# Kernel optimization log

Hardware: AMD Instinct MI355X
Metric: run time of the kernel (lower is better)

The kernel has to match this reference:

```python
import jax, jax.numpy as jnp
import numpy as np

B, NPG, HID, HEADS, L = 8, 512, 128, 8, 4
N = B * NPG
E = 16384
EDIM = HID // 4  # edge_dim = hidden_dim // 4 = 32


def _ln(x, g, b):
    m = x.mean(-1, keepdims=True)
    v = ((x - m) ** 2).mean(-1, keepdims=True)
    return (x - m) / jnp.sqrt(v + 1e-5) * g + b


def setup_inputs() -> dict:
    key = jax.random.key(0)
    ks = jax.random.split(key, 24)
    s = 0.05
    epg = E // B
    base = jnp.repeat(jnp.arange(B) * NPG, epg)
    src = base + jax.random.randint(ks[0], (E,), 0, NPG)
    dst = base + jax.random.randint(ks[1], (E,), 0, NPG)
    d = {
        'x': jax.random.randint(ks[2], (N, 1), 0, 100),
        'edge_index': jnp.stack([src, dst]),
        'edge_attr': jax.random.normal(ks[3], (E, 1), jnp.float32),
        'batch': jnp.repeat(jnp.arange(B), NPG),
        'atom_emb': jax.random.normal(ks[4], (100, HID)) * s,
        'edge_w': jax.random.normal(ks[5], (1, EDIM)) * s,
        'edge_b': jnp.zeros((EDIM,)),
        'wq': jax.random.normal(ks[6], (L, HID, HEADS * HID)) * s,
        'bq': jnp.zeros((L, HEADS * HID)),
        'wk': jax.random.normal(ks[7], (L, HID, HEADS * HID)) * s,
        'bk': jnp.zeros((L, HEADS * HID)),
        'wv': jax.random.normal(ks[8], (L, HID, HEADS * HID)) * s,
        'bv': jnp.zeros((L, HEADS * HID)),
        'we': jax.random.normal(ks[9], (L, EDIM, HEADS * HID)) * s,
        'wskip': jax.random.normal(ks[10], (L, HID, HID)) * s,
        'bskip': jnp.zeros((L, HID)),
        'ln_g': jnp.ones((L, HID)),
        'ln_b': jnp.zeros((L, HID)),
        'mha_in_w': jax.random.normal(ks[11], (HID, 3 * HID)) * s,
        'mha_in_b': jnp.zeros((3 * HID,)),
        'mha_out_w': jax.random.normal(ks[12], (HID, HID)) * s,
        'mha_out_b': jnp.zeros((HID,)),
        'w1': jax.random.normal(ks[13], (HID, HID)) * s,
        'b1': jnp.zeros((HID,)),
        'w2': jax.random.normal(ks[14], (HID, HID // 2)) * s,
        'b2': jnp.zeros((HID // 2,)),
        'w3': jax.random.normal(ks[15], (HID // 2, 3)) * s,
        'b3': jnp.zeros((3,)),
    }
    return d


def reference(x, edge_index, edge_attr, batch, atom_emb, edge_w, edge_b,
              wq, bq, wk, bk, wv, bv, we, wskip, bskip, ln_g, ln_b,
              mha_in_w, mha_in_b, mha_out_w, mha_out_b, w1, b1, w2, b2, w3, b3):
    src, dst = edge_index[0], edge_index[1]
    h = atom_emb[x[:, 0]]                       # [N, HID]
    e = edge_attr @ edge_w + edge_b             # [E, EDIM]
    scale = 1.0 / jnp.sqrt(jnp.float32(HID))    # per-head channel dim = HID
    for i in range(L):
        res = h
        q = (h @ wq[i] + bq[i]).reshape(N, HEADS, HID)
        k = (h @ wk[i] + bk[i]).reshape(N, HEADS, HID)
        v = (h @ wv[i] + bv[i]).reshape(N, HEADS, HID)
        ee = (e @ we[i]).reshape(E, HEADS, HID)
        kj = k[src] + ee                        # [E, HEADS, HID]
        vj = v[src] + ee
        logits = jnp.einsum('ehd,ehd->eh', q[dst], kj) * scale
        m = jax.ops.segment_max(logits, dst, num_segments=N)
        a = jnp.exp(logits - m[dst])
        z = jax.ops.segment_sum(a, dst, num_segments=N)
        a = a / (z[dst] + 1e-16)                # edge softmax per target node
        agg = jax.ops.segment_sum(a[:, :, None] * vj, dst, num_segments=N)
        out = agg.mean(axis=1) + h @ wskip[i] + bskip[i]  # concat=False + root skip
        h = jax.nn.gelu(_ln(out + res, ln_g[i], ln_b[i]), approximate=False)
    # equal-size graphs: ragged->padded conversion is a plain reshape, no padding
    p = h.reshape(B, NPG, HID)
    qkv = p @ mha_in_w + mha_in_b               # [B, n, 3*HID]
    hd = HID // HEADS
    q, k, v = [t.reshape(B, NPG, HEADS, hd).transpose(0, 2, 1, 3)
               for t in jnp.split(qkv, 3, axis=-1)]
    att = jax.nn.softmax(jnp.einsum('bhqd,bhkd->bhqk', q, k) / jnp.sqrt(jnp.float32(hd)), axis=-1)
    o = jnp.einsum('bhqk,bhkd->bhqd', att, v).transpose(0, 2, 1, 3).reshape(B, NPG, HID)
    o = (o @ mha_out_w + mha_out_b).reshape(N, HID)
    y = jax.nn.gelu(o @ w1 + b1, approximate=False)
    y = jax.nn.gelu(y @ w2 + b2, approximate=False)
    return y @ w3 + b3                          # [N, 3]
```

## Files before the change

### kernel.cpp

```cpp
#include <hip/hip_runtime.h>
#include <hip/hip_bf16.h>
#include <math.h>

#define NN 4096
#define NE 16384
#define NLAYERS 4

#define WT_STRIDE 442368

typedef __attribute__((ext_vector_type(8))) short bf16x8;
typedef __attribute__((ext_vector_type(4))) float floatx4;

__device__ __forceinline__ float gelu_f(float x) {
  return 0.5f * x * (1.0f + erff(x * 0.70710678118654752440f));
}

__device__ __forceinline__ void bsplit(float a, unsigned short& hi, unsigned short& lo) {
  __hip_bfloat16 h16 = __float2bfloat16(a);
  hi = *(unsigned short*)&h16;
  const float r = a - __bfloat162float(h16);
  __hip_bfloat16 l16 = __float2bfloat16(r);
  lo = *(unsigned short*)&l16;
}

union F16U { float4 v4[4]; float f[16]; };

__global__ void k_init(const int* __restrict__ x, const float* __restrict__ atom_emb,
                       const float* __restrict__ edge_attr, const float* __restrict__ edge_w,
                       const float* __restrict__ edge_b, float* __restrict__ h,
                       float* __restrict__ ef, int* __restrict__ counts,
                       unsigned short* __restrict__ hhi, unsigned short* __restrict__ hlo) {
  const int idx = blockIdx.x * 256 + threadIdx.x;
  const float hv = atom_emb[x[idx >> 7] * 128 + (idx & 127)];
  h[idx] = hv;
  bsplit(hv, hhi[idx], hlo[idx]);
  ef[idx] = edge_attr[idx >> 5] * edge_w[idx & 31] + edge_b[idx & 31];
  if (idx < NN) counts[idx] = 0;
}

__global__ void k_hist(const int* __restrict__ eidx, int* __restrict__ counts) {
  const int e = blockIdx.x * 256 + threadIdx.x;
  if (e < NE) atomicAdd(&counts[eidx[NE + e]], 1);
}

__global__ void k_scan(const int* __restrict__ counts, int* __restrict__ offs,
                       int* __restrict__ heads) {
  __shared__ int tmp[1024];
  const int t = threadIdx.x;
  const int c0 = counts[t*4], c1 = counts[t*4+1], c2 = counts[t*4+2], c3 = counts[t*4+3];
  const int s = c0 + c1 + c2 + c3;
  tmp[t] = s; __syncthreads();
  for (int off = 1; off < 1024; off <<= 1) {
    int v = (t >= off) ? tmp[t - off] : 0;
    __syncthreads();
    tmp[t] += v;
    __syncthreads();
  }
  int base = tmp[t] - s;
  offs[t*4]   = base;                heads[t*4]   = base;
  offs[t*4+1] = base + c0;           heads[t*4+1] = base + c0;
  offs[t*4+2] = base + c0 + c1;      heads[t*4+2] = base + c0 + c1;
  offs[t*4+3] = base + c0 + c1 + c2; heads[t*4+3] = base + c0 + c1 + c2;
  if (t == 1023) offs[NN] = tmp[1023];
}

__global__ void k_scatter(const int* __restrict__ eidx, int* __restrict__ heads,
                          int* __restrict__ elist) {
  const int e = blockIdx.x * 256 + threadIdx.x;
  if (e < NE) {
    int p = atomicAdd(&heads[eidx[NE + e]], 1);
    elist[p] = e;
  }
}

__global__ __launch_bounds__(256) void k_wcvt(
    const float* __restrict__ wq, const float* __restrict__ wk,
    const float* __restrict__ wv, const float* __restrict__ wsk,
    unsigned short* __restrict__ wthi, unsigned short* __restrict__ wtlo) {
  const int z = blockIdx.z;
  const int layer = z >> 2, mat = z & 3;
  int NC; const float* W; int woff;
  if (mat == 0)      { NC = 1024; W = wq  + (size_t)layer * 131072; woff = 0; }
  else if (mat == 1) { NC = 1024; W = wk  + (size_t)layer * 131072; woff = 131072; }
  else if (mat == 2) { NC = 1024; W = wv  + (size_t)layer * 131072; woff = 262144; }
  else               { NC = 128;  W = wsk + (size_t)layer * 16384;  woff = 393216; }
  const int c0 = blockIdx.x * 64;
  if (c0 >= NC) return;
  const int k0 = blockIdx.y * 64;
  __shared__ unsigned short th[64][65], tl[64][65];
  const int t = threadIdx.x;
  for (int i = t; i < 4096; i += 256) {
    const int kk = i >> 6, c = i & 63;
    bsplit(W[(size_t)(k0 + kk) * NC + c0 + c], th[kk][c], tl[kk][c]);
  }
  __syncthreads();
  unsigned short* oh = wthi + (size_t)layer * WT_STRIDE + woff;
  unsigned short* ol = wtlo + (size_t)layer * WT_STRIDE + woff;
  for (int i = t; i < 4096; i += 256) {
    const int n = i >> 6, k = i & 63;
    oh[(size_t)(c0 + n) * 128 + k0 + k] = th[k][n];
    ol[(size_t)(c0 + n) * 128 + k0 + k] = tl[k][n];
  }
}

__global__ __launch_bounds__(256) void k_wqe(
    const float* __restrict__ wq, const float* __restrict__ bq,
    const float* __restrict__ we, unsigned short* __restrict__ wthi,
    unsigned short* __restrict__ wtlo, float* __restrict__ bqe) {
  const int layer = blockIdx.x >> 3, hh = blockIdx.x & 7;
  const float* wq_l = wq + (size_t)layer * 131072;
  const float* we_l = we + (size_t)layer * 32768;
  const float* bq_l = bq + (size_t)layer * 1024;
  __shared__ float wqS[128][132];
  __shared__ float weS[32][132];
  const int t = threadIdx.x;
  for (int i = t; i < 4096; i += 256) {
    const int d = i >> 5, dd4 = (i & 31) << 2;
    *(float4*)&wqS[d][dd4] = *(const float4*)&wq_l[(size_t)d * 1024 + hh * 128 + dd4];
  }
  for (int i = t; i < 1024; i += 256) {
    const int c = i >> 5, dd4 = (i & 31) << 2;
    *(float4*)&weS[c][dd4] = *(const float4*)&we_l[(size_t)c * 1024 + hh * 128 + dd4];
  }
  __syncthreads();
  const int d = t & 127, cg = t >> 7;
  float acc[16];
  #pragma unroll
  for (int cc = 0; cc < 16; cc++) acc[cc] = 0.f;
  for (int dd = 0; dd < 128; dd++) {
    const float a = wqS[d][dd];
    #pragma unroll
    for (int cc = 0; cc < 16; cc++)
      acc[cc] += a * weS[cg * 16 + cc][dd];
  }
  unsigned short* oh = wthi + (size_t)layer * WT_STRIDE + 409600;
  unsigned short* ol = wtlo + (size_t)layer * WT_STRIDE + 409600;
  #pragma unroll
  for (int cc = 0; cc < 16; cc++) {
    const int j = hh * 32 + cg * 16 + cc;
    unsigned short hi, lo;
    bsplit(acc[cc], hi, lo);
    oh[(size_t)j * 128 + d] = hi;
    ol[(size_t)j * 128 + d] = lo;
  }
  if (t < 32) {
    float s = 0.f;
    for (int dd = 0; dd < 128; dd++) s += bq_l[hh * 128 + dd] * weS[t][dd];
    bqe[layer * 256 + hh * 32 + t] = s;
  }
}

__global__ __launch_bounds__(256) void k_mfqkv(
    const unsigned short* __restrict__ hhi, const unsigned short* __restrict__ hlo,
    const unsigned short* __restrict__ wth, const unsigned short* __restrict__ wtl,
    const float* __restrict__ bq, const float* __restrict__ bk,
    const float* __restrict__ bv, const float* __restrict__ bsk,
    const float* __restrict__ bqe_l,
    float* __restrict__ qb, float* __restrict__ kb,
    float* __restrict__ vb, float* __restrict__ skb, float* __restrict__ qeb) {
  const int xb = blockIdx.x;
  int NC; const float* bias; float* C; int woff; int c0;
  if (xb < 16)      { NC = 1024; bias = bq;    C = qb;  woff = 0;      c0 = xb * 64; }
  else if (xb < 32) { NC = 1024; bias = bk;    C = kb;  woff = 131072; c0 = (xb-16) * 64; }
  else if (xb < 48) { NC = 1024; bias = bv;    C = vb;  woff = 262144; c0 = (xb-32) * 64; }
  else if (xb < 50) { NC = 128;  bias = bsk;   C = skb; woff = 393216; c0 = (xb-48) * 64; }
  else              { NC = 256;  bias = bqe_l; C = qeb; woff = 409600; c0 = (xb-50) * 64; }
  __shared__ unsigned short Ah[64][136], Al[64][136], Wh[64][136], Wl[64][136];
  const int t = threadIdx.x;
  const int n0 = blockIdx.y * 64;
  for (int i = t; i < 1024; i += 256) {
    const int r = i >> 4, c8 = (i & 15) << 3;
    *(uint4*)&Ah[r][c8] = *(const uint4*)&hhi[(size_t)(n0 + r) * 128 + c8];
    *(uint4*)&Al[r][c8] = *(const uint4*)&hlo[(size_t)(n0 + r) * 128 + c8];
    *(uint4*)&Wh[r][c8] = *(const uint4*)&wth[woff + (size_t)(c0 + r) * 128 + c8];
    *(uint4*)&Wl[r][c8] = *(const uint4*)&wtl[woff + (size_t)(c0 + r) * 128 + c8];
  }
  __syncthreads();
  const int w = t >> 6, l = t & 63;
  const int quad = l >> 4, lm = l & 15;
  floatx4 acc[4] = {{0.f,0.f,0.f,0.f},{0.f,0.f,0.f,0.f},{0.f,0.f,0.f,0.f},{0.f,0.f,0.f,0.f}};
  #pragma unroll
  for (int kc = 0; kc < 4; kc++) {
    const int ko = kc * 32 + quad * 8;
    const bf16x8 ah = *(const bf16x8*)&Ah[w * 16 + lm][ko];
    const bf16x8 al = *(const bf16x8*)&Al[w * 16 + lm][ko];
    #pragma unroll
    for (int ct = 0; ct < 4; ct++) {
      const bf16x8 bh = *(const bf16x8*)&Wh[ct * 16 + lm][ko];
      const bf16x8 bl = *(const bf16x8*)&Wl[ct * 16 + lm][ko];
      acc[ct] = __builtin_amdgcn_mfma_f32_16x16x32_bf16(ah, bh, acc[ct], 0, 0, 0);
      acc[ct] = __builtin_amdgcn_mfma_f32_16x16x32_bf16(ah, bl, acc[ct], 0, 0, 0);
      acc[ct] = __builtin_amdgcn_mfma_f32_16x16x32_bf16(al, bh, acc[ct], 0, 0, 0);
    }
  }
  #pragma unroll
  for (int ct = 0; ct < 4; ct++) {
    const int col = c0 + ct * 16 + lm;
    const float bb = bias[col];
    #pragma unroll
    for (int r = 0; r < 4; r++) {
      const int row = n0 + w * 16 + quad * 4 + r;
      C[(size_t)row * NC + col] = acc[ct][r] + bb;
    }
  }
}

__global__ __launch_bounds__(256) void k_gemm2(const float* __restrict__ A,
                                               const float* __restrict__ W,
                                               const float* __restrict__ bias,
                                               float* __restrict__ C, int NC, int gelu) {
  __shared__ float As[128][65];
  __shared__ float Ws[128][64];
  const int t = threadIdx.x;
  const int n0 = blockIdx.y * 64, c0 = blockIdx.x * 64;
  for (int i = t; i < 2048; i += 256) {
    const int r = i & 63, k4 = (i >> 6) << 2;
    const float4 a = *(const float4*)&A[(size_t)(n0 + r) * 128 + k4];
    As[k4+0][r] = a.x; As[k4+1][r] = a.y; As[k4+2][r] = a.z; As[k4+3][r] = a.w;
  }
  for (int i = t; i < 2048; i += 256) {
    const int kk = i >> 4, c4 = (i & 15) << 2;
    *(float4*)&Ws[kk][c4] = *(const float4*)&W[(size_t)kk * NC + c0 + c4];
  }
  __syncthreads();
  const int tr = (t >> 4) << 2;
  const int tc = (t & 15) << 2;
  float acc[4][4];
  #pragma unroll
  for (int i = 0; i < 4; i++)
    #pragma unroll
    for (int j = 0; j < 4; j++) acc[i][j] = 0.f;
  #pragma unroll 8
  for (int k = 0; k < 128; k++) {
    const float4 av = *(const float4*)&As[k][tr];
    const float4 wv = *(const float4*)&Ws[k][tc];
    acc[0][0] += av.x*wv.x; acc[0][1] += av.x*wv.y; acc[0][2] += av.x*wv.z; acc[0][3] += av.x*wv.w;
    acc[1][0] += av.y*wv.x; acc[1][1] += av.y*wv.y; acc[1][2] += av.y*wv.z; acc[1][3] += av.y*wv.w;
    acc[2][0] += av.z*wv.x; acc[2][1] += av.z*wv.y; acc[2][2] += av.z*wv.z; acc[2][3] += av.z*wv.w;
    acc[3][0] += av.w*wv.x; acc[3][1] += av.w*wv.y; acc[3][2] += av.w*wv.z; acc[3][3] += av.w*wv.w;
  }
  const float4 bb = *(const float4*)&bias[c0 + tc];
  #pragma unroll
  for (int i = 0; i < 4; i++) {
    float4 v;
    v.x = acc[i][0] + bb.x; v.y = acc[i][1] + bb.y;
    v.z = acc[i][2] + bb.z; v.w = acc[i][3] + bb.w;
    if (gelu) { v.x = gelu_f(v.x); v.y = gelu_f(v.y); v.z = gelu_f(v.z); v.w = gelu_f(v.w); }
    *(float4*)&C[(size_t)(n0 + tr + i) * NC + c0 + tc] = v;
  }
}

__global__ __launch_bounds__(512) void k_edgepost(
    const float* __restrict__ qb, const float* __restrict__ kb,
    const float* __restrict__ vb, const float* __restrict__ qe,
    const float* __restrict__ ef, const int* __restrict__ offs,
    const int* __restrict__ elist, const int* __restrict__ eidx,
    const float* __restrict__ we_l, const float* __restrict__ skb,
    const float* __restrict__ lng, const float* __restrict__ lnb,
    float* __restrict__ h,
    unsigned short* __restrict__ hhi, unsigned short* __restrict__ hlo) {
  __shared__ float Ss[8][256];
  __shared__ float Am[8][128];
  const int t = threadIdx.x;
  const int wid = t >> 6, lane = t & 63;
  const int n0 = (blockIdx.x & 7) * 512 + (blockIdx.x >> 3) * 8;
  const int n = n0 + wid;
  {
    const int hh = lane >> 3, s8 = lane & 7;
    const int d0 = hh * 128 + s8 * 16;
    F16U qv;
    {
      const float4* qp = (const float4*)(qb + (size_t)n * 1024 + d0);
      #pragma unroll
      for (int i = 0; i < 4; i++) qv.v4[i] = qp[i];
    }
    const float4 qe4 = *(const float4*)(qe + (size_t)n * 256 + hh * 32 + s8 * 4);
    float m = -INFINITY, z = 0.f;
    float acc[16];
    #pragma unroll
    for (int i = 0; i < 16; i++) acc[i] = 0.f;
    float sx = 0.f, sy = 0.f, sz = 0.f, sw = 0.f;
    const int e0 = offs[n], e1 = offs[n + 1];
    for (int tt = e0; tt < e1; tt++) {
      const int e = elist[tt];
      const int src = eidx[e];
      F16U kv;
      {
        const float4* kp = (const float4*)(kb + (size_t)src * 1024 + d0);
        #pragma unroll
        for (int i = 0; i < 4; i++) kv.v4[i] = kp[i];
      }
      const float4 ef4 = *(const float4*)(ef + (size_t)e * 32 + s8 * 4);
      float p0 = qe4.x*ef4.x + qe4.y*ef4.y;
      float p1 = qe4.z*ef4.z + qe4.w*ef4.w;
      float p2 = 0.f, p3 = 0.f;
      #pragma unroll
      for (int i = 0; i < 4; i++) {
        p0 += qv.f[i]      * kv.f[i];
        p1 += qv.f[4 + i]  * kv.f[4 + i];
        p2 += qv.f[8 + i]  * kv.f[8 + i];
        p3 += qv.f[12 + i] * kv.f[12 + i];
      }
      float p = (p0 + p1) + (p2 + p3);
      p += __shfl_xor(p, 1);
      p += __shfl_xor(p, 2);
      p += __shfl_xor(p, 4);
      const float logit = p * 0.08838834764831845f;
      if (logit > m + 8.f) {
        const float f = __expf(m - logit);
        z *= f; sx *= f; sy *= f; sz *= f; sw *= f;
        #pragma unroll
        for (int i = 0; i < 16; i++) acc[i] *= f;
        m = logit;
      }
      const float w = __expf(logit - m);
      z += w;
      F16U vv;
      {
        const float4* vp = (const float4*)(vb + (size_t)src * 1024 + d0);
        #pragma unroll
        for (int i = 0; i < 4; i++) vv.v4[i] = vp[i];
      }
      #pragma unroll
      for (int i = 0; i < 16; i++) acc[i] += w * vv.f[i];
      sx += w * ef4.x; sy += w * ef4.y;
      sz += w * ef4.z; sw += w * ef4.w;
    }
    const float inv = 1.f / (z + 1e-16f);
    *(float4*)&Ss[wid][hh * 32 + s8 * 4] =
        make_float4(sx * inv, sy * inv, sz * inv, sw * inv);
    F16U ov;
    #pragma unroll
    for (int i = 0; i < 16; i++) ov.f[i] = acc[i] * inv;
    #pragma unroll
    for (int mask = 8; mask <= 32; mask <<= 1)
      #pragma unroll
      for (int i = 0; i < 16; i++) ov.f[i] += __shfl_xor(ov.f[i], mask);
    if (hh == 0) {
      #pragma unroll
      for (int i = 0; i < 16; i++) ov.f[i] *= 0.125f;
      #pragma unroll
      for (int i = 0; i < 4; i++)
        *(float4*)&Am[wid][s8 * 16 + i * 4] = ov.v4[i];
    }
  }
  __syncthreads();
  {
    const int col = t & 127, grp = t >> 7;
    float acc0 = 0.f, acc1 = 0.f;
    const float* wp = we_l + col;
    #pragma unroll
    for (int hh2 = 0; hh2 < 8; hh2++) {
      #pragma unroll 4
      for (int c = 0; c < 32; c++) {
        const float wv = wp[(size_t)c * 1024 + hh2 * 128];
        const int k = hh2 * 32 + c;
        acc0 += Ss[grp * 2 + 0][k] * wv;
        acc1 += Ss[grp * 2 + 1][k] * wv;
      }
    }
    const int nA = grp * 2, nB = grp * 2 + 1;
    const size_t oA = (size_t)(n0 + nA) * 128 + col;
    const size_t oB = (size_t)(n0 + nB) * 128 + col;
    Am[nA][col] = Am[nA][col] + 0.125f * acc0 + skb[oA] + h[oA];
    Am[nB][col] = Am[nB][col] + 0.125f * acc1 + skb[oB] + h[oB];
  }
  __syncthreads();
  {
    const float v0 = Am[wid][lane], v1 = Am[wid][lane + 64];
    float s = v0 + v1;
    #pragma unroll
    for (int mask = 1; mask <= 32; mask <<= 1) s += __shfl_xor(s, mask);
    const float mean = s * (1.f / 128.f);
    const float d0 = v0 - mean, d1 = v1 - mean;
    float q = d0 * d0 + d1 * d1;
    #pragma unroll
    for (int mask = 1; mask <= 32; mask <<= 1) q += __shfl_xor(q, mask);
    const float rstd = 1.f / sqrtf(q * (1.f / 128.f) + 1e-5f);
    const float y0 = d0 * rstd * lng[lane] + lnb[lane];
    const float y1 = d1 * rstd * lng[lane + 64] + lnb[lane + 64];
    const float r0 = gelu_f(y0);
    const float r1 = gelu_f(y1);
    const size_t o = (size_t)n * 128 + lane;
    h[o] = r0;
    h[o + 64] = r1;
    bsplit(r0, hhi[o], hlo[o]);
    bsplit(r1, hhi[o + 64], hlo[o + 64]);
  }
}

__global__ __launch_bounds__(256) void k_attn2b(const float* __restrict__ qkvm,
                                                float* __restrict__ pm,
                                                float* __restrict__ pz,
                                                float* __restrict__ pacc) {
  __shared__ float ks2[64][16];
  __shared__ float vs2[64][16];
  const int ksp = blockIdx.x, qt = blockIdx.y, bh = blockIdx.z;
  const int b = bh >> 3, hh = bh & 7;
  const int t = threadIdx.x;
  const size_t rbase = (size_t)(b * 512 + ksp * 64);
  {
    const int j = t >> 2, d4 = (t & 3) << 2;
    const size_t ro = (rbase + j) * 384 + hh * 16 + d4;
    *(float4*)&ks2[j][d4] = *(const float4*)&qkvm[ro + 128];
    *(float4*)&vs2[j][d4] = *(const float4*)&qkvm[ro + 256];
  }
  __syncthreads();
  const int qrow = qt * 256 + t;
  const int nq = b * 512 + qrow;
  F16U qv;
  {
    const float4* qp = (const float4*)(qkvm + (size_t)nq * 384 + hh * 16);
    #pragma unroll
    for (int i = 0; i < 4; i++) qv.v4[i] = qp[i];
  }
  float m = -INFINITY, z = 0.f;
  float acc[16];
  #pragma unroll
  for (int i = 0; i < 16; i++) acc[i] = 0.f;
  for (int j = 0; j < 64; j += 2) {
    F16U k0, k1, v0, v1;
    {
      const float4* p0 = (const float4*)ks2[j];
      const float4* p1 = (const float4*)ks2[j + 1];
      const float4* q0 = (const float4*)vs2[j];
      const float4* q1 = (const float4*)vs2[j + 1];
      #pragma unroll
      for (int i = 0; i < 4; i++) {
        k0.v4[i] = p0[i]; k1.v4[i] = p1[i];
        v0.v4[i] = q0[i]; v1.v4[i] = q1[i];
      }
    }
    float a0 = 0.f, a1 = 0.f, a2 = 0.f, a3 = 0.f;
    float b0 = 0.f, b1 = 0.f, b2 = 0.f, b3 = 0.f;
    #pragma unroll
    for (int i = 0; i < 4; i++) {
      a0 += qv.f[i]      * k0.f[i];
      a1 += qv.f[4 + i]  * k0.f[4 + i];
      a2 += qv.f[8 + i]  * k0.f[8 + i];
      a3 += qv.f[12 + i] * k0.f[12 + i];
      b0 += qv.f[i]      * k1.f[i];
      b1 += qv.f[4 + i]  * k1.f[4 + i];
      b2 += qv.f[8 + i]  * k1.f[8 + i];
      b3 += qv.f[12 + i] * k1.f[12 + i];
    }
    const float sa = ((a0 + a1) + (a2 + a3)) * 0.25f;
    const float sb = ((b0 + b1) + (b2 + b3)) * 0.25f;
    const float smax = fmaxf(sa, sb);
    if (smax > m + 8.f) {
      const float f = __expf(m - smax);
      z *= f;
      #pragma unroll
      for (int i = 0; i < 16; i++) acc[i] *= f;
      m = smax;
    }
    const float wa = __expf(sa - m);
    const float wb = __expf(sb - m);
    z += wa + wb;
    #pragma unroll
    for (int i = 0; i < 16; i++)
      acc[i] += wa * v0.f[i] + wb * v1.f[i];
  }
  const int p = (bh * 512 + qrow) * 8 + ksp;
  pm[p] = m; pz[p] = z;
  float4* pp = (float4*)&pacc[(size_t)p * 16];
  F16U ov;
  #pragma unroll
  for (int i = 0; i < 16; i++) ov.f[i] = acc[i];
  #pragma unroll
  for (int i = 0; i < 4; i++) pp[i] = ov.v4[i];
}

__global__ __launch_bounds__(256) void k_tail(
    const float* __restrict__ pm, const float* __restrict__ pz,
    const float* __restrict__ pacc,
    const float* __restrict__ mha_out_w, const float* __restrict__ mha_out_b,
    const float* __restrict__ w1, const float* __restrict__ b1,
    const float* __restrict__ w2, const float* __restrict__ b2,
    const float* __restrict__ w3, const float* __restrict__ b3,
    float* __restrict__ out) {
  __shared__ float RA[4][128];
  __shared__ float RB[4][128];
  const int t = threadIdx.x;
  const int w = t >> 6, lane = t & 63;
  const int n = blockIdx.x * 4 + w;
  const int b = n >> 9, qrow = n & 511;
  #pragma unroll
  for (int half = 0; half < 2; half++) {
    const int c = lane + half * 64;
    const int hh = c >> 4, d = c & 15;
    const int base = ((b * 8 + hh) * 512 + qrow) * 8;
    float ms = pm[base];
    #pragma unroll
    for (int s = 1; s < 8; s++) ms = fmaxf(ms, pm[base + s]);
    float z = 0.f, o = 0.f;
    #pragma unroll
    for (int s = 0; s < 8; s++) {
      const float wg = __expf(pm[base + s] - ms);
      z += pz[base + s] * wg;
      o += pacc[(size_t)(base + s) * 16 + d] * wg;
    }
    RA[w][c] = o / z;
  }
  __syncthreads();
  {
    float a0 = 0.f, a1 = 0.f;
    #pragma unroll 8
    for (int k = 0; k < 128; k++) {
      const float r = RA[w][k];
      a0 += r * mha_out_w[k * 128 + lane];
      a1 += r * mha_out_w[k * 128 + lane + 64];
    }
    RB[w][lane]      = a0 + mha_out_b[lane];
    RB[w][lane + 64] = a1 + mha_out_b[lane + 64];
  }
  __syncthreads();
  {
    float a0 = 0.f, a1 = 0.f;
    #pragma unroll 8
    for (int k = 0; k < 128; k++) {
      const float r = RB[w][k];
      a0 += r * w1[k * 128 + lane];
      a1 += r * w1[k * 128 + lane + 64];
    }
    RA[w][lane]      = gelu_f(a0 + b1[lane]);
    RA[w][lane + 64] = gelu_f(a1 + b1[lane + 64]);
  }
  __syncthreads();
  {
    float a0 = 0.f;
    #pragma unroll 8
    for (int k = 0; k < 128; k++)
      a0 += RA[w][k] * w2[k * 64 + lane];
    RB[w][lane] = gelu_f(a0 + b2[lane]);
  }
  __syncthreads();
  if (lane < 3) {
    float s = b3[lane];
    for (int c = 0; c < 64; c++) s += RB[w][c] * w3[c * 3 + lane];
    out[(size_t)n * 3 + lane] = s;
  }
}

extern "C" void kernel_launch(void* const* d_in, const int* in_sizes, int n_in,
                              void* d_out, int out_size, void* d_ws, size_t ws_size,
                              hipStream_t stream) {
  const int*   x         = (const int*)d_in[0];
  const int*   eidx      = (const int*)d_in[1];
  const float* edge_attr = (const float*)d_in[2];
  const float* atom_emb  = (const float*)d_in[4];
  const float* edge_w    = (const float*)d_in[5];
  const float* edge_b    = (const float*)d_in[6];
  const float* wq        = (const float*)d_in[7];
  const float* bq        = (const float*)d_in[8];
  const float* wk        = (const float*)d_in[9];
  const float* bk        = (const float*)d_in[10];
  const float* wv        = (const float*)d_in[11];
  const float* bv        = (const float*)d_in[12];
  const float* we        = (const float*)d_in[13];
  const float* wskip     = (const float*)d_in[14];
  const float* bskip     = (const float*)d_in[15];
  const float* ln_g      = (const float*)d_in[16];
  const float* ln_b      = (const float*)d_in[17];
  const float* mha_in_w  = (const float*)d_in[18];
  const float* mha_in_b  = (const float*)d_in[19];
  const float* mha_out_w = (const float*)d_in[20];
  const float* mha_out_b = (const float*)d_in[21];
  const float* w1        = (const float*)d_in[22];
  const float* b1        = (const float*)d_in[23];
  const float* w2        = (const float*)d_in[24];
  const float* b2        = (const float*)d_in[25];
  const float* w3        = (const float*)d_in[26];
  const float* b3        = (const float*)d_in[27];

  float* ws   = (float*)d_ws;
  float* h    = ws;
  float* ef   = h + 524288;
  float* qb   = ef + 524288;
  float* kb   = qb + 4194304;
  float* vb   = kb + 4194304;
  float* qe   = vb + 4194304;
  float* big  = qe + 1048576;
  float* skb  = big + 1048576;
  unsigned short* hhi  = (unsigned short*)(big + 1572864);
  unsigned short* hlo  = hhi + 524288;
  unsigned short* wthi = hlo + 524288;
  unsigned short* wtlo = wthi + 1769472;
  float* sbuf = big + 4194304;
  float* qkvm = qb;
  float* pm   = sbuf;
  float* pz   = sbuf + 262144;
  float* pacc = big;
  int* counts = (int*)(sbuf + 1048576);
  int* offs   = counts + 4100;
  int* heads  = offs + 4100;
  int* elist  = heads + 4100;
  float* bqe  = (float*)(elist + 16384);

  k_init<<<2048, 256, 0, stream>>>(x, atom_emb, edge_attr, edge_w, edge_b, h, ef, counts,
                                   hhi, hlo);
  k_hist<<<64, 256, 0, stream>>>(eidx, counts);
  k_scan<<<1, 1024, 0, stream>>>(counts, offs, heads);
  k_scatter<<<64, 256, 0, stream>>>(eidx, heads, elist);
  k_wcvt<<<dim3(16, 2, 16), 256, 0, stream>>>(wq, wk, wv, wskip, wthi, wtlo);
  k_wqe<<<32, 256, 0, stream>>>(wq, bq, we, wthi, wtlo, bqe);

  for (int i = 0; i < NLAYERS; i++) {
    const float* bq_i  = bq + (size_t)i * 1024;
    const float* bk_i  = bk + (size_t)i * 1024;
    const float* bv_i  = bv + (size_t)i * 1024;
    const float* we_i  = we + (size_t)i * 32768;
    const float* bsk_i = bskip + (size_t)i * 128;
    const float* g_i   = ln_g + (size_t)i * 128;
    const float* b_i   = ln_b + (size_t)i * 128;
    const unsigned short* wth_i = wthi + (size_t)i * WT_STRIDE;
    const unsigned short* wtl_i = wtlo + (size_t)i * WT_STRIDE;

    k_mfqkv<<<dim3(54, 64), 256, 0, stream>>>(hhi, hlo, wth_i, wtl_i,
                                              bq_i, bk_i, bv_i, bsk_i, bqe + i * 256,
                                              qb, kb, vb, skb, qe);
    k_edgepost<<<512, 512, 0, stream>>>(qb, kb, vb, qe, ef, offs, elist, eidx,
                                        we_i, skb, g_i, b_i, h, hhi, hlo);
  }

  k_gemm2<<<dim3(6, 64), 256, 0, stream>>>(h, mha_in_w, mha_in_b, qkvm, 384, 0);
  k_attn2b<<<dim3(8, 2, 64), 256, 0, stream>>>(qkvm, pm, pz, pacc);
  k_tail<<<1024, 256, 0, stream>>>(pm, pz, pacc,
                                   mha_out_w, mha_out_b, w1, b1, w2, b2, w3, b3,
                                   (float*)d_out);
}
```

Measured before the change: 478.7 us.

## Fuse CSR scatter into scan, split attention keys finer, tile tail MLP weights

Merges the edge scatter into the single-block scan kernel, using shared-memory atomics for the per-node heads and dropping one launch. Doubles the attention key-split count (16 chunks of 32 keys) to raise block count and parallelism, at the cost of more partial results for the tail to merge. Restructures the tail MLP so each block handles 8 rows and stages weight tiles in shared memory, reusing each weight load across two rows per warp. Partial buffers move to the kb region to fit the larger split.

```diff
diff --git a/kernel.cpp b/kernel.cpp
--- a/kernel.cpp
+++ b/kernel.cpp
@@ -43,9 +43,10 @@
   if (e < NE) atomicAdd(&counts[eidx[NE + e]], 1);
 }
 
-__global__ void k_scan(const int* __restrict__ counts, int* __restrict__ offs,
-                       int* __restrict__ heads) {
+__global__ void k_scan2(const int* __restrict__ counts, int* __restrict__ offs,
+                        const int* __restrict__ eidx, int* __restrict__ elist) {
   __shared__ int tmp[1024];
+  __shared__ int sheads[4096];
   const int t = threadIdx.x;
   const int c0 = counts[t*4], c1 = counts[t*4+1], c2 = counts[t*4+2], c3 = counts[t*4+3];
   const int s = c0 + c1 + c2 + c3;
@@ -57,18 +58,14 @@
     __syncthreads();
   }
   int base = tmp[t] - s;
-  offs[t*4]   = base;                heads[t*4]   = base;
-  offs[t*4+1] = base + c0;           heads[t*4+1] = base + c0;
-  offs[t*4+2] = base + c0 + c1;      heads[t*4+2] = base + c0 + c1;
-  offs[t*4+3] = base + c0 + c1 + c2; heads[t*4+3] = base + c0 + c1 + c2;
+  offs[t*4]   = base;                sheads[t*4]   = base;
+  offs[t*4+1] = base + c0;           sheads[t*4+1] = base + c0;
+  offs[t*4+2] = base + c0 + c1;      sheads[t*4+2] = base + c0 + c1;
+  offs[t*4+3] = base + c0 + c1 + c2; sheads[t*4+3] = base + c0 + c1 + c2;
   if (t == 1023) offs[NN] = tmp[1023];
-}
-
-__global__ void k_scatter(const int* __restrict__ eidx, int* __restrict__ heads,
-                          int* __restrict__ elist) {
-  const int e = blockIdx.x * 256 + threadIdx.x;
-  if (e < NE) {
-    int p = atomicAdd(&heads[eidx[NE + e]], 1);
+  __syncthreads();
+  for (int e = t; e < NE; e += 1024) {
+    const int p = atomicAdd(&sheads[eidx[NE + e]], 1);
     elist[p] = e;
   }
 }
@@ -393,17 +390,17 @@
                                                 float* __restrict__ pm,
                                                 float* __restrict__ pz,
                                                 float* __restrict__ pacc) {
-  __shared__ float ks2[64][16];
-  __shared__ float vs2[64][16];
+  __shared__ float ks2[32][16];
+  __shared__ float vs2[32][16];
   const int ksp = blockIdx.x, qt = blockIdx.y, bh = blockIdx.z;
   const int b = bh >> 3, hh = bh & 7;
   const int t = threadIdx.x;
-  const size_t rbase = (size_t)(b * 512 + ksp * 64);
-  {
-    const int j = t >> 2, d4 = (t & 3) << 2;
+  const size_t rbase = (size_t)(b * 512 + ksp * 32);
+  {
+    const int j = (t & 127) >> 2, d4 = (t & 3) << 2;
     const size_t ro = (rbase + j) * 384 + hh * 16 + d4;
-    *(float4*)&ks2[j][d4] = *(const float4*)&qkvm[ro + 128];
-    *(float4*)&vs2[j][d4] = *(const float4*)&qkvm[ro + 256];
+    if (t < 128) *(float4*)&ks2[j][d4] = *(const float4*)&qkvm[ro + 128];
+    else         *(float4*)&vs2[j][d4] = *(const float4*)&qkvm[ro + 256];
   }
   __syncthreads();
   const int qrow = qt * 256 + t;
@@ -418,7 +415,7 @@
   float acc[16];
   #pragma unroll
   for (int i = 0; i < 16; i++) acc[i] = 0.f;
-  for (int j = 0; j < 64; j += 2) {
+  for (int j = 0; j < 32; j += 2) {
     F16U k0, k1, v0, v1;
     {
       const float4* p0 = (const float4*)ks2[j];
@@ -461,7 +458,7 @@
     for (int i = 0; i < 16; i++)
       acc[i] += wa * v0.f[i] + wb * v1.f[i];
   }
-  const int p = (bh * 512 + qrow) * 8 + ksp;
+  const int p = (bh * 512 + qrow) * 16 + ksp;
   pm[p] = m; pz[p] = z;
   float4* pp = (float4*)&pacc[(size_t)p * 16];
   F16U ov;
@@ -479,66 +476,121 @@
     const float* __restrict__ w2, const float* __restrict__ b2,
     const float* __restrict__ w3, const float* __restrict__ b3,
     float* __restrict__ out) {
-  __shared__ float RA[4][128];
-  __shared__ float RB[4][128];
+  __shared__ float R0[8][128];
+  __shared__ float R1[8][128];
+  __shared__ float Wc[32][128];
   const int t = threadIdx.x;
   const int w = t >> 6, lane = t & 63;
-  const int n = blockIdx.x * 4 + w;
-  const int b = n >> 9, qrow = n & 511;
-  #pragma unroll
-  for (int half = 0; half < 2; half++) {
-    const int c = lane + half * 64;
-    const int hh = c >> 4, d = c & 15;
-    const int base = ((b * 8 + hh) * 512 + qrow) * 8;
-    float ms = pm[base];
-    #pragma unroll
-    for (int s = 1; s < 8; s++) ms = fmaxf(ms, pm[base + s]);
-    float z = 0.f, o = 0.f;
-    #pragma unroll
-    for (int s = 0; s < 8; s++) {
-      const float wg = __expf(pm[base + s] - ms);
-      z += pz[base + s] * wg;
-      o += pacc[(size_t)(base + s) * 16 + d] * wg;
-    }
-    RA[w][c] = o / z;
-  }
-  __syncthreads();
+  const int n0 = blockIdx.x * 8;
+  const int r0i = w * 2, r1i = w * 2 + 1;
+  #pragma unroll
+  for (int rr = 0; rr < 2; rr++) {
+    const int n = n0 + w * 2 + rr;
+    const int b = n >> 9, qrow = n & 511;
+    #pragma unroll
+    for (int half = 0; half < 2; half++) {
+      const int c = lane + half * 64;
+      const int hh = c >> 4, d = c & 15;
+      const int base = ((b * 8 + hh) * 512 + qrow) * 16;
+      float ms = pm[base];
+      #pragma unroll
+      for (int s = 1; s < 16; s++) ms = fmaxf(ms, pm[base + s]);
+      float z = 0.f, o = 0.f;
+      #pragma unroll
+      for (int s = 0; s < 16; s++) {
+        const float wg = __expf(pm[base + s] - ms);
+        z += pz[base + s] * wg;
+        o += pacc[(size_t)(base + s) * 16 + d] * wg;
+      }
+      R0[w * 2 + rr][c] = o / z;
+    }
+  }
+  {
+    float a00 = 0.f, a01 = 0.f, a10 = 0.f, a11 = 0.f;
+    for (int kc = 0; kc < 4; kc++) {
+      __syncthreads();
+      #pragma unroll
+      for (int i = 0; i < 4; i++) {
+        const int idx = i * 256 + t, kk = idx >> 5, c4 = (idx & 31) << 2;
+        *(float4*)&Wc[kk][c4] = *(const float4*)&mha_out_w[(size_t)(kc*32 + kk) * 128 + c4];
+      }
+      __syncthreads();
+      for (int k4 = 0; k4 < 32; k4 += 4) {
+        const float4 rv0 = *(const float4*)&R0[r0i][kc*32 + k4];
+        const float4 rv1 = *(const float4*)&R0[r1i][kc*32 + k4];
+        #pragma unroll
+        for (int j = 0; j < 4; j++) {
+          const float wv0 = Wc[k4 + j][lane], wv1 = Wc[k4 + j][lane + 64];
+          const float rr0 = ((const float*)&rv0)[j], rr1 = ((const float*)&rv1)[j];
+          a00 += rr0 * wv0; a01 += rr0 * wv1;
+          a10 += rr1 * wv0; a11 += rr1 * wv1;
+        }
+      }
+    }
+    R1[r0i][lane]      = a00 + mha_out_b[lane];
+    R1[r0i][lane + 64] = a01 + mha_out_b[lane + 64];
+    R1[r1i][lane]      = a10 + mha_out_b[lane];
+    R1[r1i][lane + 64] = a11 + mha_out_b[lane + 64];
+  }
+  {
+    float a00 = 0.f, a01 = 0.f, a10 = 0.f, a11 = 0.f;
+    for (int kc = 0; kc < 4; kc++) {
+      __syncthreads();
+      #pragma unroll
+      for (int i = 0; i < 4; i++) {
+        const int idx = i * 256 + t, kk = idx >> 5, c4 = (idx & 31) << 2;
+        *(float4*)&Wc[kk][c4] = *(const float4*)&w1[(size_t)(kc*32 + kk) * 128 + c4];
+      }
+      __syncthreads();
+      for (int k4 = 0; k4 < 32; k4 += 4) {
+        const float4 rv0 = *(const float4*)&R1[r0i][kc*32 + k4];
+        const float4 rv1 = *(const float4*)&R1[r1i][kc*32 + k4];
+        #pragma unroll
+        for (int j = 0; j < 4; j++) {
+          const float wv0 = Wc[k4 + j][lane], wv1 = Wc[k4 + j][lane + 64];
+          const float rr0 = ((const float*)&rv0)[j], rr1 = ((const float*)&rv1)[j];
+          a00 += rr0 * wv0; a01 += rr0 * wv1;
+          a10 += rr1 * wv0; a11 += rr1 * wv1;
+        }
+      }
+    }
+    R0[r0i][lane]      = gelu_f(a00 + b1[lane]);
+    R0[r0i][lane + 64] = gelu_f(a01 + b1[lane + 64]);
+    R0[r1i][lane]      = gelu_f(a10 + b1[lane]);
+    R0[r1i][lane + 64] = gelu_f(a11 + b1[lane + 64]);
+  }
   {
     float a0 = 0.f, a1 = 0.f;
-    #pragma unroll 8
-    for (int k = 0; k < 128; k++) {
-      const float r = RA[w][k];
-      a0 += r * mha_out_w[k * 128 + lane];
-      a1 += r * mha_out_w[k * 128 + lane + 64];
-    }
-    RB[w][lane]      = a0 + mha_out_b[lane];
-    RB[w][lane + 64] = a1 + mha_out_b[lane + 64];
-  }
-  __syncthreads();
-  {
-    float a0 = 0.f, a1 = 0.f;
-    #pragma unroll 8
-    for (int k = 0; k < 128; k++) {
-      const float r = RB[w][k];
-      a0 += r * w1[k * 128 + lane];
-      a1 += r * w1[k * 128 + lane + 64];
-    }
-    RA[w][lane]      = gelu_f(a0 + b1[lane]);
-    RA[w][lane + 64] = gelu_f(a1 + b1[lane + 64]);
-  }
-  __syncthreads();
-  {
-    float a0 = 0.f;
-    #pragma unroll 8
-    for (int k = 0; k < 128; k++)
-      a0 += RA[w][k] * w2[k * 64 + lane];
-    RB[w][lane] = gelu_f(a0 + b2[lane]);
-  }
-  __syncthreads();
+    for (int kc = 0; kc < 4; kc++) {
+      __syncthreads();
+      #pragma unroll
+      for (int i = 0; i < 2; i++) {
+        const int idx = i * 256 + t, kk = idx >> 4, c4 = (idx & 15) << 2;
+        *(float4*)&Wc[kk][c4] = *(const float4*)&w2[(size_t)(kc*32 + kk) * 64 + c4];
+      }
+      __syncthreads();
+      for (int k4 = 0; k4 < 32; k4 += 4) {
+        const float4 rv0 = *(const float4*)&R0[r0i][kc*32 + k4];
+        const float4 rv1 = *(const float4*)&R0[r1i][kc*32 + k4];
+        #pragma unroll
+        for (int j = 0; j < 4; j++) {
+          const float wv = Wc[k4 + j][lane];
+          a0 += ((const float*)&rv0)[j] * wv;
+          a1 += ((const float*)&rv1)[j] * wv;
+        }
+      }
+    }
+    R1[r0i][lane] = gelu_f(a0 + b2[lane]);
+    R1[r1i][lane] = gelu_f(a1 + b2[lane]);
+  }
   if (lane < 3) {
-    float s = b3[lane];
-    for (int c = 0; c < 64; c++) s += RB[w][c] * w3[c * 3 + lane];
-    out[(size_t)n * 3 + lane] = s;
+    #pragma unroll
+    for (int rr = 0; rr < 2; rr++) {
+      const int row = w * 2 + rr;
+      float s = b3[lane];
+      for (int c = 0; c < 64; c++) s += R1[row][c] * w3[c * 3 + lane];
+      out[(size_t)(n0 + row) * 3 + lane] = s;
+    }
   }
 }
 
@@ -589,8 +641,8 @@
   float* sbuf = big + 4194304;
   float* qkvm = qb;
   float* pm   = sbuf;
-  float* pz   = sbuf + 262144;
-  float* pacc = big;
+  float* pz   = sbuf + 524288;
+  float* pacc = kb;
   int* counts = (int*)(sbuf + 1048576);
   int* offs   = counts + 4100;
   int* heads  = offs + 4100;
@@ -600,8 +652,7 @@
   k_init<<<2048, 256, 0, stream>>>(x, atom_emb, edge_attr, edge_w, edge_b, h, ef, counts,
                                    hhi, hlo);
   k_hist<<<64, 256, 0, stream>>>(eidx, counts);
-  k_scan<<<1, 1024, 0, stream>>>(counts, offs, heads);
-  k_scatter<<<64, 256, 0, stream>>>(eidx, heads, elist);
+  k_scan2<<<1, 1024, 0, stream>>>(counts, offs, eidx, elist);
   k_wcvt<<<dim3(16, 2, 16), 256, 0, stream>>>(wq, wk, wv, wskip, wthi, wtlo);
   k_wqe<<<32, 256, 0, stream>>>(wq, bq, we, wthi, wtlo, bqe);
 
@@ -624,8 +675,8 @@
   }
 
   k_gemm2<<<dim3(6, 64), 256, 0, stream>>>(h, mha_in_w, mha_in_b, qkvm, 384, 0);
-  k_attn2b<<<dim3(8, 2, 64), 256, 0, stream>>>(qkvm, pm, pz, pacc);
-  k_tail<<<1024, 256, 0, stream>>>(pm, pz, pacc,
-                                   mha_out_w, mha_out_b, w1, b1, w2, b2, w3, b3,
-                                   (float*)d_out);
-}
+  k_attn2b<<<dim3(16, 2, 64), 256, 0, stream>>>(qkvm, pm, pz, pacc);
+  k_tail<<<512, 256, 0, stream>>>(pm, pz, pacc,
+                                  mha_out_w, mha_out_b, w1, b1, w2, b2, w3, b3,
+                                  (float*)d_out);
+}
```

Result: slower. 521.7 us (+9.0%).

## Fuse CSR scan with scatter and register-block MLP tail over transposed weights

Applied to the files above, without the earlier changes.

The scan kernel now also scatters edges into the CSR list, using bucket heads kept in shared memory, which removes one launch and the global atomics. A new setup kernel stores transposed copies of the MHA out-projection, w1 and w2. The tail kernel then has each wave handle two rows, reads weight rows as float4 and reuses each weight load for both rows. Block-level barriers in the tail are dropped because each wave only touches its own rows. The per-lane strided reads of the transposed weights are not coalesced and depend on cache hits.

```diff
diff --git a/kernel.cpp b/kernel.cpp
--- a/kernel.cpp
+++ b/kernel.cpp
@@ -43,9 +43,10 @@
   if (e < NE) atomicAdd(&counts[eidx[NE + e]], 1);
 }
 
-__global__ void k_scan(const int* __restrict__ counts, int* __restrict__ offs,
-                       int* __restrict__ heads) {
+__global__ void k_scan2(const int* __restrict__ counts, int* __restrict__ offs,
+                        const int* __restrict__ eidx, int* __restrict__ elist) {
   __shared__ int tmp[1024];
+  __shared__ int sheads[4096];
   const int t = threadIdx.x;
   const int c0 = counts[t*4], c1 = counts[t*4+1], c2 = counts[t*4+2], c3 = counts[t*4+3];
   const int s = c0 + c1 + c2 + c3;
@@ -57,18 +58,14 @@
     __syncthreads();
   }
   int base = tmp[t] - s;
-  offs[t*4]   = base;                heads[t*4]   = base;
-  offs[t*4+1] = base + c0;           heads[t*4+1] = base + c0;
-  offs[t*4+2] = base + c0 + c1;      heads[t*4+2] = base + c0 + c1;
-  offs[t*4+3] = base + c0 + c1 + c2; heads[t*4+3] = base + c0 + c1 + c2;
+  offs[t*4]   = base;                sheads[t*4]   = base;
+  offs[t*4+1] = base + c0;           sheads[t*4+1] = base + c0;
+  offs[t*4+2] = base + c0 + c1;      sheads[t*4+2] = base + c0 + c1;
+  offs[t*4+3] = base + c0 + c1 + c2; sheads[t*4+3] = base + c0 + c1 + c2;
   if (t == 1023) offs[NN] = tmp[1023];
-}
-
-__global__ void k_scatter(const int* __restrict__ eidx, int* __restrict__ heads,
-                          int* __restrict__ elist) {
-  const int e = blockIdx.x * 256 + threadIdx.x;
-  if (e < NE) {
-    int p = atomicAdd(&heads[eidx[NE + e]], 1);
+  __syncthreads();
+  for (int e = t; e < NE; e += 1024) {
+    const int p = atomicAdd(&sheads[eidx[NE + e]], 1);
     elist[p] = e;
   }
 }
@@ -147,6 +144,21 @@
     float s = 0.f;
     for (int dd = 0; dd < 128; dd++) s += bq_l[hh * 128 + dd] * weS[t][dd];
     bqe[layer * 256 + hh * 32 + t] = s;
+  }
+}
+
+__global__ void k_wt(const float* __restrict__ mo, const float* __restrict__ w1,
+                     const float* __restrict__ w2, float* __restrict__ wtT) {
+  const int idx = blockIdx.x * 256 + threadIdx.x;
+  if (idx < 16384) {
+    const int c = idx >> 7, k = idx & 127;
+    wtT[idx] = mo[k * 128 + c];
+  } else if (idx < 32768) {
+    const int j = idx - 16384, c = j >> 7, k = j & 127;
+    wtT[idx] = w1[k * 128 + c];
+  } else if (idx < 40960) {
+    const int j = idx - 32768, c = j >> 7, k = j & 127;
+    wtT[idx] = w2[k * 64 + c];
   }
 }
 
@@ -473,72 +485,101 @@
 
 __global__ __launch_bounds__(256) void k_tail(
     const float* __restrict__ pm, const float* __restrict__ pz,
-    const float* __restrict__ pacc,
-    const float* __restrict__ mha_out_w, const float* __restrict__ mha_out_b,
-    const float* __restrict__ w1, const float* __restrict__ b1,
-    const float* __restrict__ w2, const float* __restrict__ b2,
+    const float* __restrict__ pacc, const float* __restrict__ wtT,
+    const float* __restrict__ mha_out_b, const float* __restrict__ b1,
+    const float* __restrict__ b2,
     const float* __restrict__ w3, const float* __restrict__ b3,
     float* __restrict__ out) {
-  __shared__ float RA[4][128];
-  __shared__ float RB[4][128];
+  __shared__ float RA[8][128];
+  __shared__ float RB[8][128];
   const int t = threadIdx.x;
   const int w = t >> 6, lane = t & 63;
-  const int n = blockIdx.x * 4 + w;
-  const int b = n >> 9, qrow = n & 511;
-  #pragma unroll
-  for (int half = 0; half < 2; half++) {
-    const int c = lane + half * 64;
-    const int hh = c >> 4, d = c & 15;
-    const int base = ((b * 8 + hh) * 512 + qrow) * 8;
-    float ms = pm[base];
-    #pragma unroll
-    for (int s = 1; s < 8; s++) ms = fmaxf(ms, pm[base + s]);
-    float z = 0.f, o = 0.f;
-    #pragma unroll
-    for (int s = 0; s < 8; s++) {
-      const float wg = __expf(pm[base + s] - ms);
-      z += pz[base + s] * wg;
-      o += pacc[(size_t)(base + s) * 16 + d] * wg;
-    }
-    RA[w][c] = o / z;
-  }
-  __syncthreads();
-  {
+  const int n0 = blockIdx.x * 8;
+  const int rA = w * 2, rB = w * 2 + 1;
+  #pragma unroll
+  for (int rr = 0; rr < 2; rr++) {
+    const int n = n0 + w * 2 + rr;
+    const int b = n >> 9, qrow = n & 511;
+    #pragma unroll
+    for (int half = 0; half < 2; half++) {
+      const int c = lane + half * 64;
+      const int hh = c >> 4, d = c & 15;
+      const int base = ((b * 8 + hh) * 512 + qrow) * 8;
+      float ms = pm[base];
+      #pragma unroll
+      for (int s = 1; s < 8; s++) ms = fmaxf(ms, pm[base + s]);
+      float z = 0.f, o = 0.f;
+      #pragma unroll
+      for (int s = 0; s < 8; s++) {
+        const float wg = __expf(pm[base + s] - ms);
+        z += pz[base + s] * wg;
+        o += pacc[(size_t)(base + s) * 16 + d] * wg;
+      }
+      RA[w * 2 + rr][c] = o / z;
+    }
+  }
+  {
+    const float4* w0p = (const float4*)&wtT[(size_t)lane * 128];
+    const float4* w1p = (const float4*)&wtT[(size_t)(lane + 64) * 128];
+    float a00 = 0.f, a01 = 0.f, a10 = 0.f, a11 = 0.f;
+    #pragma unroll 8
+    for (int k4 = 0; k4 < 32; k4++) {
+      const float4 wv0 = w0p[k4];
+      const float4 wv1 = w1p[k4];
+      const float4 r0 = *(const float4*)&RA[rA][k4 * 4];
+      const float4 r1 = *(const float4*)&RA[rB][k4 * 4];
+      a00 += r0.x*wv0.x + r0.y*wv0.y + r0.z*wv0.z + r0.w*wv0.w;
+      a01 += r0.x*wv1.x + r0.y*wv1.y + r0.z*wv1.z + r0.w*wv1.w;
+      a10 += r1.x*wv0.x + r1.y*wv0.y + r1.z*wv0.z + r1.w*wv0.w;
+      a11 += r1.x*wv1.x + r1.y*wv1.y + r1.z*wv1.z + r1.w*wv1.w;
+    }
+    RB[rA][lane]      = a00 + mha_out_b[lane];
+    RB[rA][lane + 64] = a01 + mha_out_b[lane + 64];
+    RB[rB][lane]      = a10 + mha_out_b[lane];
+    RB[rB][lane + 64] = a11 + mha_out_b[lane + 64];
+  }
+  {
+    const float4* w0p = (const float4*)&wtT[16384 + (size_t)lane * 128];
+    const float4* w1p = (const float4*)&wtT[16384 + (size_t)(lane + 64) * 128];
+    float a00 = 0.f, a01 = 0.f, a10 = 0.f, a11 = 0.f;
+    #pragma unroll 8
+    for (int k4 = 0; k4 < 32; k4++) {
+      const float4 wv0 = w0p[k4];
+      const float4 wv1 = w1p[k4];
+      const float4 r0 = *(const float4*)&RB[rA][k4 * 4];
+      const float4 r1 = *(const float4*)&RB[rB][k4 * 4];
+      a00 += r0.x*wv0.x + r0.y*wv0.y + r0.z*wv0.z + r0.w*wv0.w;
+      a01 += r0.x*wv1.x + r0.y*wv1.y + r0.z*wv1.z + r0.w*wv1.w;
+      a10 += r1.x*wv0.x + r1.y*wv0.y + r1.z*wv0.z + r1.w*wv0.w;
+      a11 += r1.x*wv1.x + r1.y*wv1.y + r1.z*wv1.z + r1.w*wv1.w;
+    }
+    RA[rA][lane]      = gelu_f(a00 + b1[lane]);
+    RA[rA][lane + 64] = gelu_f(a01 + b1[lane + 64]);
+    RA[rB][lane]      = gelu_f(a10 + b1[lane]);
+    RA[rB][lane + 64] = gelu_f(a11 + b1[lane + 64]);
+  }
+  {
+    const float4* w0p = (const float4*)&wtT[32768 + (size_t)lane * 128];
     float a0 = 0.f, a1 = 0.f;
     #pragma unroll 8
-    for (int k = 0; k < 128; k++) {
-      const float r = RA[w][k];
-      a0 += r * mha_out_w[k * 128 + lane];
-      a1 += r * mha_out_w[k * 128 + lane + 64];
-    }
-    RB[w][lane]      = a0 + mha_out_b[lane];
-    RB[w][lane + 64] = a1 + mha_out_b[lane + 64];
-  }
-  __syncthreads();
-  {
-    float a0 = 0.f, a1 = 0.f;
-    #pragma unroll 8
-    for (int k = 0; k < 128; k++) {
-      const float r = RB[w][k];
-      a0 += r * w1[k * 128 + lane];
-      a1 += r * w1[k * 128 + lane + 64];
-    }
-    RA[w][lane]      = gelu_f(a0 + b1[lane]);
-    RA[w][lane + 64] = gelu_f(a1 + b1[lane + 64]);
-  }
-  __syncthreads();
-  {
-    float a0 = 0.f;
-    #pragma unroll 8
-    for (int k = 0; k < 128; k++)
-      a0 += RA[w][k] * w2[k * 64 + lane];
-    RB[w][lane] = gelu_f(a0 + b2[lane]);
-  }
-  __syncthreads();
+    for (int k4 = 0; k4 < 32; k4++) {
+      const float4 wv = w0p[k4];
+      const float4 r0 = *(const float4*)&RA[rA][k4 * 4];
+      const float4 r1 = *(const float4*)&RA[rB][k4 * 4];
+      a0 += r0.x*wv.x + r0.y*wv.y + r0.z*wv.z + r0.w*wv.w;
+      a1 += r1.x*wv.x + r1.y*wv.y + r1.z*wv.z + r1.w*wv.w;
+    }
+    RB[rA][lane] = gelu_f(a0 + b2[lane]);
+    RB[rB][lane] = gelu_f(a1 + b2[lane]);
+  }
   if (lane < 3) {
-    float s = b3[lane];
-    for (int c = 0; c < 64; c++) s += RB[w][c] * w3[c * 3 + lane];
-    out[(size_t)n * 3 + lane] = s;
+    #pragma unroll
+    for (int rr = 0; rr < 2; rr++) {
+      const int row = w * 2 + rr;
+      float s = b3[lane];
+      for (int c = 0; c < 64; c++) s += RB[row][c] * w3[c * 3 + lane];
+      out[(size_t)(n0 + row) * 3 + lane] = s;
+    }
   }
 }
 
@@ -596,14 +637,15 @@
   int* heads  = offs + 4100;
   int* elist  = heads + 4100;
   float* bqe  = (float*)(elist + 16384);
+  float* wtT  = bqe + 1024;
 
   k_init<<<2048, 256, 0, stream>>>(x, atom_emb, edge_attr, edge_w, edge_b, h, ef, counts,
                                    hhi, hlo);
   k_hist<<<64, 256, 0, stream>>>(eidx, counts);
-  k_scan<<<1, 1024, 0, stream>>>(counts, offs, heads);
-  k_scatter<<<64, 256, 0, stream>>>(eidx, heads, elist);
+  k_scan2<<<1, 1024, 0, stream>>>(counts, offs, eidx, elist);
   k_wcvt<<<dim3(16, 2, 16), 256, 0, stream>>>(wq, wk, wv, wskip, wthi, wtlo);
   k_wqe<<<32, 256, 0, stream>>>(wq, bq, we, wthi, wtlo, bqe);
+  k_wt<<<160, 256, 0, stream>>>(mha_out_w, w1, w2, wtT);
 
   for (int i = 0; i < NLAYERS; i++) {
     const float* bq_i  = bq + (size_t)i * 1024;
@@ -625,7 +667,7 @@
 
   k_gemm2<<<dim3(6, 64), 256, 0, stream>>>(h, mha_in_w, mha_in_b, qkvm, 384, 0);
   k_attn2b<<<dim3(8, 2, 64), 256, 0, stream>>>(qkvm, pm, pz, pacc);
-  k_tail<<<1024, 256, 0, stream>>>(pm, pz, pacc,
-                                   mha_out_w, mha_out_b, w1, b1, w2, b2, w3, b3,
-                                   (float*)d_out);
-}
+  k_tail<<<512, 256, 0, stream>>>(pm, pz, pacc, wtT,
+                                  mha_out_b, b1, b2, w3, b3,
+                                  (float*)d_out);
+}
```

Measured after the change: 501.9 us. +4.9%, slower.
